# Performance work log

Measured on AMD Instinct MI355X. Metric: run time of the kernel, lower is better.

Reference implementation:

```python
import jax, jax.numpy as jnp
import numpy as np

N = 50000      # nodes
E = 800000     # edges (before self loops)
IN = 128       # in_channels
HID = 128      # 2*out_channels
OUT = 64       # out_channels
NEG_SLOPE = 0.2


def _gat_conv(x, src, dst, W, a_src, a_dst, b, n_nodes):
    """Single-head PyG GATConv (concat=True, heads=1, self-loops already added)."""
    h = x @ W                                   # [N, F]
    alpha_s = h @ a_src                         # [N]
    alpha_d = h @ a_dst                         # [N]
    e = alpha_s[src] + alpha_d[dst]             # [E'] logits per edge j->i
    e = jnp.where(e > 0, e, NEG_SLOPE * e)      # LeakyReLU(0.2)
    # segment softmax over destination node
    m = jax.ops.segment_max(e, dst, num_segments=n_nodes)   # [N]
    w = jnp.exp(e - m[dst])                                   # [E']
    denom = jax.ops.segment_sum(w, dst, num_segments=n_nodes) # [N]
    alpha = w / denom[dst]                                     # [E']
    out = jax.ops.segment_sum(alpha[:, None] * h[src], dst, num_segments=n_nodes)
    return out + b


def _with_self_loops(edge_index, n_nodes):
    loop = jnp.arange(n_nodes, dtype=edge_index.dtype)
    src = jnp.concatenate([edge_index[0], loop])
    dst = jnp.concatenate([edge_index[1], loop])
    return src, dst


def setup_inputs() -> dict:
    key = jax.random.key(0)
    ks = jax.random.split(key, 10)
    s = 0.1
    return {
        "x": jax.random.normal(ks[0], (N, IN), jnp.float32),
        "edge_index": jax.random.randint(ks[1], (2, E), 0, N, jnp.int32),
        "W1": jax.random.normal(ks[2], (IN, HID), jnp.float32) * s,
        "a1_src": jax.random.normal(ks[3], (HID,), jnp.float32) * s,
        "a1_dst": jax.random.normal(ks[4], (HID,), jnp.float32) * s,
        "b1": jnp.zeros((HID,), jnp.float32),
        "W2": jax.random.normal(ks[5], (HID, OUT), jnp.float32) * s,
        "a2_src": jax.random.normal(ks[6], (OUT,), jnp.float32) * s,
        "a2_dst": jax.random.normal(ks[7], (OUT,), jnp.float32) * s,
        "b2": jnp.zeros((OUT,), jnp.float32),
    }


def reference(x, edge_index, W1, a1_src, a1_dst, b1, W2, a2_src, a2_dst, b2):
    src, dst = _with_self_loops(edge_index, N)
    h = _gat_conv(x, src, dst, W1, a1_src, a1_dst, b1, N)
    h = jax.nn.relu(h)
    return _gat_conv(h, src, dst, W2, a2_src, a2_dst, b2, N)
```

## Files before the change

### kernel.cpp

```cpp
#include <hip/hip_runtime.h>
#include <hip/hip_bf16.h>


#define BCAP 4096

typedef __attribute__((ext_vector_type(8))) short bf16x8;
typedef __attribute__((ext_vector_type(4))) float f32x4;

__device__ __forceinline__ unsigned short bf16bits(float f){
  __hip_bfloat16 b = __float2bfloat16(f);
  return *(unsigned short*)&b;
}
__device__ __forceinline__ float bf16lo(unsigned int v){ return __uint_as_float(v << 16); }
__device__ __forceinline__ float bf16hi(unsigned int v){ return __uint_as_float(v & 0xFFFF0000u); }

__global__ __launch_bounds__(256) void prep_all(
    const float* __restrict__ W1, const float* __restrict__ W2,
    const float* __restrict__ a2s, const float* __restrict__ a2d,
    unsigned short* __restrict__ W1t, unsigned short* __restrict__ W2t,
    float* __restrict__ vas, float* __restrict__ vad,
    int* __restrict__ bucketCount)
{
  int b = blockIdx.x, t = threadIdx.x;
  if (b < 48){
    int idx = b*256 + t;
    if (idx < 8192){
      int n = idx >> 6, k2 = idx & 63;
      float a = W1[(size_t)(2*k2)*128 + n];
      float c = W1[(size_t)(2*k2+1)*128 + n];
      ushort2 o; o.x = bf16bits(a); o.y = bf16bits(c);
      *(ushort2*)&W1t[(size_t)n*128 + 2*k2] = o;
    } else {
      int r = idx - 8192;
      int n = r >> 6, k2 = r & 63;
      float a = W2[(size_t)(2*k2)*64 + n];
      float c = W2[(size_t)(2*k2+1)*64 + n];
      ushort2 o; o.x = bf16bits(a); o.y = bf16bits(c);
      *(ushort2*)&W2t[(size_t)n*128 + 2*k2] = o;
    }
  } else if (b == 48){
    int k = t & 127;
    const float* av = (t < 128) ? a2s : a2d;
    float* ov = (t < 128) ? vas : vad;
    float s = 0.f;
    for (int n=0; n<64; n++) s += W2[(size_t)k*64 + n] * av[n];
    ov[k] = s;
  } else {
    bucketCount[t] = 0; bucketCount[t+256] = 0;
  }
}

template<int NC, bool FUSE>
__device__ __forceinline__ void gemm_body(
    const float* __restrict__ Af, const unsigned short* __restrict__ Ah,
    const unsigned short* __restrict__ Wt,
    const float* __restrict__ avs, const float* __restrict__ avd,
    unsigned short* __restrict__ H, float* __restrict__ as_, float* __restrict__ ad_,
    int M, int rowBase, unsigned short* As, unsigned short* Ws)
{
  const int K = 128;
  int t = threadIdx.x;
  if (Af){
    #pragma unroll
    for (int i=0;i<8;i++){
      int idx = t + i*256; int r = idx>>5, k4 = idx&31;
      int grow = rowBase + r;
      float4 v = (grow<M) ? *(const float4*)&Af[(size_t)grow*K + k4*4]
                          : make_float4(0.f,0.f,0.f,0.f);
      ushort4 o; o.x=bf16bits(v.x); o.y=bf16bits(v.y); o.z=bf16bits(v.z); o.w=bf16bits(v.w);
      *(ushort4*)&As[r*136 + k4*4] = o;
    }
  } else {
    #pragma unroll
    for (int i=0;i<4;i++){
      int idx = t + i*256; int r = idx>>4, k8 = idx&15;
      int grow = rowBase + r;
      uint4 v = (grow<M) ? *(const uint4*)&Ah[(size_t)grow*K + k8*8]
                         : make_uint4(0u,0u,0u,0u);
      *(uint4*)&As[r*136 + k8*8] = v;
    }
  }
  int wave = t>>6, lane = t&63, ln = lane&15, q = lane>>4;
  f32x4 acc[NC/16];
  #pragma unroll
  for (int nt=0; nt<NC/16; nt++) acc[nt] = (f32x4){0.f,0.f,0.f,0.f};

  #pragma unroll
  for (int ch=0; ch<NC/64; ++ch){
    __syncthreads();
    #pragma unroll
    for (int i=0;i<4;i++){
      int idx = t + i*256; int n = idx>>4, k8 = idx&15;
      *(uint4*)&Ws[n*136 + k8*8] = *(const uint4*)&Wt[(size_t)(ch*64+n)*K + k8*8];
    }
    __syncthreads();
    #pragma unroll
    for (int kk=0;kk<4;kk++){
      bf16x8 a = *(const bf16x8*)&As[(wave*16+ln)*136 + kk*32 + q*8];
      #pragma unroll
      for (int nt=0; nt<4; nt++){
        bf16x8 b = *(const bf16x8*)&Ws[(nt*16+ln)*136 + kk*32 + q*8];
        acc[ch*4+nt] = __builtin_amdgcn_mfma_f32_16x16x32_bf16(a, b, acc[ch*4+nt], 0, 0, 0);
      }
    }
  }
  float asl[NC/16], adl[NC/16];
  if (FUSE){
    #pragma unroll
    for (int nt=0; nt<NC/16; nt++){ asl[nt]=avs[nt*16+ln]; adl[nt]=avd[nt*16+ln]; }
  }
  #pragma unroll
  for (int i=0;i<4;i++){
    int grow = rowBase + wave*16 + q*4 + i;
    if (grow < M){
      float ps=0.f, pd=0.f;
      #pragma unroll
      for (int nt=0; nt<NC/16; nt++){
        float v = acc[nt][i];
        H[(size_t)grow*NC + nt*16 + ln] = bf16bits(v);
        if (FUSE){ ps += v*asl[nt]; pd += v*adl[nt]; }
      }
      if (FUSE){
        #pragma unroll
        for (int d=1; d<16; d<<=1){ ps += __shfl_xor(ps,d); pd += __shfl_xor(pd,d); }
        if (ln==0){ as_[grow] = ps; ad_[grow] = pd; }
      }
    }
  }
}

__global__ __launch_bounds__(256) void scatter_or_gemm(
    const int* __restrict__ src, const int* __restrict__ dst,
    int* __restrict__ bucketCount, unsigned int* __restrict__ gbuf, int E, int SB,
    const float* __restrict__ x, const unsigned short* __restrict__ W1t,
    const float* __restrict__ a1s, const float* __restrict__ a1d,
    unsigned short* __restrict__ h1, float* __restrict__ as1, float* __restrict__ ad1,
    int M)
{
  __shared__ unsigned short smem[64*136 + 64*136];
  int t = threadIdx.x;
  if ((int)blockIdx.x >= SB){
    gemm_body<128, true>(x, nullptr, W1t, a1s, a1d, h1, as1, ad1, M,
                         (blockIdx.x - SB)*64, smem, smem + 64*136);
    return;
  }
  int* hist = (int*)smem;
  int* base = hist + 512;
  int e0 = blockIdx.x * 4096;
  hist[t] = 0; hist[t+256] = 0;
  __syncthreads();
  int sv[16], dv[16];
  #pragma unroll
  for (int k=0;k<16;k++){
    int i = e0 + t + k*256;
    if (i < E){ sv[k]=src[i]; dv[k]=dst[i]; atomicAdd(&hist[dv[k]>>7], 1); }
    else { sv[k] = -1; dv[k] = 0; }
  }
  __syncthreads();
  int h0 = hist[t], h1c = hist[t+256];
  if (h0 > 0)  base[t]     = atomicAdd(&bucketCount[t],     h0);
  if (h1c > 0) base[t+256] = atomicAdd(&bucketCount[t+256], h1c);
  __syncthreads();
  hist[t] = 0; hist[t+256] = 0;
  __syncthreads();
  #pragma unroll
  for (int k=0;k<16;k++){
    if (sv[k] >= 0){
      int b = dv[k] >> 7;
      int r = base[b] + atomicAdd(&hist[b], 1);
      if (r < BCAP)
        gbuf[(size_t)b*BCAP + r] = ((unsigned)(dv[k] & 127) << 16) | (unsigned)sv[k];
    }
  }
}

__global__ __launch_bounds__(512) void fine_sort(
    const unsigned int* __restrict__ gbuf, const int* __restrict__ bucketCount,
    int* __restrict__ offs, int* __restrict__ srcS, int N, int E, int B)
{
  __shared__ int sh[512];
  __shared__ int h[128];
  __shared__ int pre[128];
  __shared__ int rank[128];
  int b = blockIdx.x, t = threadIdx.x;
  {
    int nd_t = 0;
    if (t < B){ int lo=t*128; nd_t = (N-lo<128)?(N-lo):128; }
    sh[t] = (t < B ? bucketCount[t] : 0) + nd_t;
    __syncthreads();
    for (int d=1; d<512; d<<=1){
      int x = (t >= d) ? sh[t-d] : 0;
      __syncthreads();
      sh[t] += x;
      __syncthreads();
    }
  }
  int cnt = bucketCount[b]; if (cnt > BCAP) cnt = BCAP;
  int lo = b*128;
  int nd = (N - lo < 128) ? (N - lo) : 128;
  int base = sh[b] - (cnt + nd);
  if (b == 0 && t == 0) offs[N] = E + N;
  if (t < 128){ h[t] = 0; rank[t] = 0; }
  __syncthreads();
  for (int i = t; i < cnt; i += 512)
    atomicAdd(&h[(gbuf[(size_t)b*BCAP + i] >> 16) & 127], 1);
  __syncthreads();
  if (t < 128) pre[t] = (t < nd) ? (h[t] + 1) : 0;
  __syncthreads();
  for (int d=1; d<128; d<<=1){
    int x = (t >= d && t < 128) ? pre[t-d] : 0;
    __syncthreads();
    if (t < 128) pre[t] += x;
    __syncthreads();
  }
  int seg = (t < nd) ? (h[t] + 1) : 0;
  int ex  = (t < 128) ? (pre[t] - seg) : 0;
  if (t < nd){
    offs[lo + t] = base + ex;
    srcS[base + ex] = lo + t;
  }
  __syncthreads();
  if (t < 128) pre[t] = ex;
  __syncthreads();
  for (int i = t; i < cnt; i += 512){
    unsigned e = gbuf[(size_t)b*BCAP + i];
    int dl = (e >> 16) & 127;
    int s  = e & 0xFFFF;
    int r  = atomicAdd(&rank[dl], 1);
    srcS[base + pre[dl] + 1 + r] = s;
  }
}

__global__ __launch_bounds__(256) void edge_agg128(
    const int* __restrict__ offs, const int* __restrict__ srcS,
    const float* __restrict__ asrc, const float* __restrict__ adst,
    const unsigned short* __restrict__ Hin, const float* __restrict__ bias,
    unsigned short* __restrict__ outp,
    const float* __restrict__ vas, const float* __restrict__ vad,
    float* __restrict__ as2, float* __restrict__ ad2, int n)
{
  int wid  = (blockIdx.x * 256 + threadIdx.x) >> 6;
  int lane = threadIdx.x & 63;
  if (wid >= n) return;
  int beg = offs[wid], end = offs[wid+1];
  float ad = adst[wid];
  int qw = lane >> 4, ql = lane & 15;
  float acc[8] = {}; float denom = 0.f;
  for (int base = beg; base < end; base += 64){
    int m = end - base; if (m > 64) m = 64;
    int   sv = (lane < m) ? srcS[base + lane] : 0;
    float av = (lane < m) ? asrc[sv] : 0.f;
    float ev = av + ad;
    ev = (ev > 0.f) ? ev : 0.2f*ev;
    float wv = (lane < m) ? __expf(ev) : 0.f;
    int j = 0;
    for (; j + 16 <= m; j += 16){
      int i0 = j+qw, i1 = j+4+qw, i2 = j+8+qw, i3 = j+12+qw;
      int   s0 = __shfl(sv,i0), s1 = __shfl(sv,i1), s2 = __shfl(sv,i2), s3 = __shfl(sv,i3);
      float w0 = __shfl(wv,i0), w1 = __shfl(wv,i1), w2 = __shfl(wv,i2), w3 = __shfl(wv,i3);
      uint4 ha = *(const uint4*)&Hin[(size_t)s0*128 + ql*8];
      uint4 hb = *(const uint4*)&Hin[(size_t)s1*128 + ql*8];
      uint4 hc = *(const uint4*)&Hin[(size_t)s2*128 + ql*8];
      uint4 hd = *(const uint4*)&Hin[(size_t)s3*128 + ql*8];
      denom += (w0 + w1) + (w2 + w3);
      acc[0]+=w0*bf16lo(ha.x)+w1*bf16lo(hb.x)+w2*bf16lo(hc.x)+w3*bf16lo(hd.x);
      acc[1]+=w0*bf16hi(ha.x)+w1*bf16hi(hb.x)+w2*bf16hi(hc.x)+w3*bf16hi(hd.x);
      acc[2]+=w0*bf16lo(ha.y)+w1*bf16lo(hb.y)+w2*bf16lo(hc.y)+w3*bf16lo(hd.y);
      acc[3]+=w0*bf16hi(ha.y)+w1*bf16hi(hb.y)+w2*bf16hi(hc.y)+w3*bf16hi(hd.y);
      acc[4]+=w0*bf16lo(ha.z)+w1*bf16lo(hb.z)+w2*bf16lo(hc.z)+w3*bf16lo(hd.z);
      acc[5]+=w0*bf16hi(ha.z)+w1*bf16hi(hb.z)+w2*bf16hi(hc.z)+w3*bf16hi(hd.z);
      acc[6]+=w0*bf16lo(ha.w)+w1*bf16lo(hb.w)+w2*bf16lo(hc.w)+w3*bf16lo(hd.w);
      acc[7]+=w0*bf16hi(ha.w)+w1*bf16hi(hb.w)+w2*bf16hi(hc.w)+w3*bf16hi(hd.w);
    }
    for (; j < m; j += 4){
      int i0 = j + qw;
      int   s0 = __shfl(sv, i0);
      float w0 = __shfl(wv, i0);
      uint4 ha = *(const uint4*)&Hin[(size_t)s0*128 + ql*8];
      denom += w0;
      acc[0]+=w0*bf16lo(ha.x); acc[1]+=w0*bf16hi(ha.x);
      acc[2]+=w0*bf16lo(ha.y); acc[3]+=w0*bf16hi(ha.y);
      acc[4]+=w0*bf16lo(ha.z); acc[5]+=w0*bf16hi(ha.z);
      acc[6]+=w0*bf16lo(ha.w); acc[7]+=w0*bf16hi(ha.w);
    }
  }
  denom += __shfl_xor(denom,16); denom += __shfl_xor(denom,32);
  #pragma unroll
  for (int k=0;k<8;k++){ acc[k]+=__shfl_xor(acc[k],16); acc[k]+=__shfl_xor(acc[k],32); }
  if (qw == 0){
    float inv = 1.0f / denom;
    float ps = 0.f, pd = 0.f;
    unsigned short o[8];
    #pragma unroll
    for (int k=0;k<8;k++){
      float v = fmaxf(acc[k]*inv + bias[ql*8+k], 0.f);
      o[k] = bf16bits(v);
      ps += v * vas[ql*8+k];
      pd += v * vad[ql*8+k];
    }
    *(uint4*)&outp[(size_t)wid*128 + ql*8] = *(uint4*)o;
    #pragma unroll
    for (int d=1; d<16; d<<=1){ ps += __shfl_xor(ps,d); pd += __shfl_xor(pd,d); }
    if (ql == 0){ as2[wid] = ps; ad2[wid] = pd; }
  }
}

__global__ __launch_bounds__(256) void gemm2_k(
    const unsigned short* __restrict__ A, const unsigned short* __restrict__ Wt,
    unsigned short* __restrict__ H, int M)
{
  __shared__ unsigned short smem[64*136 + 64*136];
  gemm_body<64, false>(nullptr, A, Wt, nullptr, nullptr, H, nullptr, nullptr,
                       M, blockIdx.x*64, smem, smem + 64*136);
}

__global__ __launch_bounds__(256) void edge_agg64(
    const int* __restrict__ offs, const int* __restrict__ srcS,
    const float* __restrict__ asrc, const float* __restrict__ adst,
    const unsigned short* __restrict__ Hin, const float* __restrict__ bias,
    float* __restrict__ outp, int n)
{
  int wid  = (blockIdx.x * 256 + threadIdx.x) >> 6;
  int lane = threadIdx.x & 63;
  if (wid >= n) return;
  int beg = offs[wid], end = offs[wid+1];
  float ad = adst[wid];
  int ew = lane >> 3, el = lane & 7;
  float acc[8] = {}; float denom = 0.f;
  for (int base = beg; base < end; base += 64){
    int m = end - base; if (m > 64) m = 64;
    int   sv = (lane < m) ? srcS[base + lane] : 0;
    float av = (lane < m) ? asrc[sv] : 0.f;
    float ev = av + ad;
    ev = (ev > 0.f) ? ev : 0.2f*ev;
    float wv = (lane < m) ? __expf(ev) : 0.f;
    int j = 0;
    for (; j + 32 <= m; j += 32){
      int i0 = j+ew, i1 = j+8+ew, i2 = j+16+ew, i3 = j+24+ew;
      int   s0 = __shfl(sv,i0), s1 = __shfl(sv,i1), s2 = __shfl(sv,i2), s3 = __shfl(sv,i3);
      float w0 = __shfl(wv,i0), w1 = __shfl(wv,i1), w2 = __shfl(wv,i2), w3 = __shfl(wv,i3);
      uint4 ha = *(const uint4*)&Hin[(size_t)s0*64 + el*8];
      uint4 hb = *(const uint4*)&Hin[(size_t)s1*64 + el*8];
      uint4 hc = *(const uint4*)&Hin[(size_t)s2*64 + el*8];
      uint4 hd = *(const uint4*)&Hin[(size_t)s3*64 + el*8];
      denom += (w0 + w1) + (w2 + w3);
      acc[0]+=w0*bf16lo(ha.x)+w1*bf16lo(hb.x)+w2*bf16lo(hc.x)+w3*bf16lo(hd.x);
      acc[1]+=w0*bf16hi(ha.x)+w1*bf16hi(hb.x)+w2*bf16hi(hc.x)+w3*bf16hi(hd.x);
      acc[2]+=w0*bf16lo(ha.y)+w1*bf16lo(hb.y)+w2*bf16lo(hc.y)+w3*bf16lo(hd.y);
      acc[3]+=w0*bf16hi(ha.y)+w1*bf16hi(hb.y)+w2*bf16hi(hc.y)+w3*bf16hi(hd.y);
      acc[4]+=w0*bf16lo(ha.z)+w1*bf16lo(hb.z)+w2*bf16lo(hc.z)+w3*bf16lo(hd.z);
      acc[5]+=w0*bf16hi(ha.z)+w1*bf16hi(hb.z)+w2*bf16hi(hc.z)+w3*bf16hi(hd.z);
      acc[6]+=w0*bf16lo(ha.w)+w1*bf16lo(hb.w)+w2*bf16lo(hc.w)+w3*bf16lo(hd.w);
      acc[7]+=w0*bf16hi(ha.w)+w1*bf16hi(hb.w)+w2*bf16hi(hc.w)+w3*bf16hi(hd.w);
    }
    for (; j < m; j += 8){
      int i0 = j + ew;
      int   s0 = __shfl(sv, i0);
      float w0 = __shfl(wv, i0);
      uint4 ha = *(const uint4*)&Hin[(size_t)s0*64 + el*8];
      denom += w0;
      acc[0]+=w0*bf16lo(ha.x); acc[1]+=w0*bf16hi(ha.x);
      acc[2]+=w0*bf16lo(ha.y); acc[3]+=w0*bf16hi(ha.y);
      acc[4]+=w0*bf16lo(ha.z); acc[5]+=w0*bf16hi(ha.z);
      acc[6]+=w0*bf16lo(ha.w); acc[7]+=w0*bf16hi(ha.w);
    }
  }
  denom += __shfl_xor(denom,8); denom += __shfl_xor(denom,16); denom += __shfl_xor(denom,32);
  #pragma unroll
  for (int k=0;k<8;k++){
    acc[k]+=__shfl_xor(acc[k],8); acc[k]+=__shfl_xor(acc[k],16); acc[k]+=__shfl_xor(acc[k],32);
  }
  if (ew == 0){
    float inv = 1.0f / denom;
    float4 o0, o1;
    o0.x = acc[0]*inv + bias[el*8+0]; o0.y = acc[1]*inv + bias[el*8+1];
    o0.z = acc[2]*inv + bias[el*8+2]; o0.w = acc[3]*inv + bias[el*8+3];
    o1.x = acc[4]*inv + bias[el*8+4]; o1.y = acc[5]*inv + bias[el*8+5];
    o1.z = acc[6]*inv + bias[el*8+6]; o1.w = acc[7]*inv + bias[el*8+7];
    *(float4*)&outp[(size_t)wid*64 + el*8]     = o0;
    *(float4*)&outp[(size_t)wid*64 + el*8 + 4] = o1;
  }
}

extern "C" void kernel_launch(void* const* d_in, const int* in_sizes, int n_in,
                              void* d_out, int out_size, void* d_ws, size_t ws_size,
                              hipStream_t stream) {
  const int IN = 128, HID = 128, OUT = 64;
  const int N = in_sizes[0] / IN;
  const int E = in_sizes[1] / 2;
  const int B = (N + 127) / 128;
  const int SB = (E + 4095) / 4096;

  const float* x    = (const float*)d_in[0];
  const int*   ei   = (const int*)d_in[1];
  const float* W1   = (const float*)d_in[2];
  const float* a1s  = (const float*)d_in[3];
  const float* a1d  = (const float*)d_in[4];
  const float* b1   = (const float*)d_in[5];
  const float* W2   = (const float*)d_in[6];
  const float* a2s  = (const float*)d_in[7];
  const float* a2d  = (const float*)d_in[8];
  const float* b2   = (const float*)d_in[9];
  float* out = (float*)d_out;

  char* w = (char*)d_ws;
  unsigned short* W1t = (unsigned short*)w; w += (size_t)HID*IN*2;
  unsigned short* W2t = (unsigned short*)w; w += (size_t)OUT*HID*2;
  unsigned short* h1    = (unsigned short*)w; w += (size_t)N*128*2;
  unsigned short* hrelu = (unsigned short*)w; w += (size_t)N*128*2;
  unsigned short* h2 = h1;
  float* as1   = (float*)w; w += (size_t)N*4;
  float* ad1   = (float*)w; w += (size_t)N*4;
  float* as2   = (float*)w; w += (size_t)N*4;
  float* ad2   = (float*)w; w += (size_t)N*4;
  float* vas   = (float*)w; w += 128*4;
  float* vad   = (float*)w; w += 128*4;
  int* offs    = (int*)w;   w += (size_t)(N+1)*4;
  int* bucketCount = (int*)w; w += 512*4;
  int* srcS    = (int*)w;   w += (size_t)(E+N)*4;
  unsigned int* gbuf = (unsigned int*)w; w += (size_t)B*BCAP*4;

  const int* esrc = ei;
  const int* edst = ei + E;

  hipLaunchKernelGGL(prep_all, dim3(50), dim3(256), 0, stream,
                     W1, W2, a2s, a2d, W1t, W2t, vas, vad, bucketCount);
  hipLaunchKernelGGL(scatter_or_gemm, dim3(SB + (N+63)/64), dim3(256), 0, stream,
                     esrc, edst, bucketCount, gbuf, E, SB,
                     x, W1t, a1s, a1d, h1, as1, ad1, N);
  hipLaunchKernelGGL(fine_sort, dim3(B), dim3(512), 0, stream,
                     gbuf, bucketCount, offs, srcS, N, E, B);
  hipLaunchKernelGGL(edge_agg128, dim3((N*64+255)/256), dim3(256), 0, stream,
                     offs, srcS, as1, ad1, h1, b1, hrelu, vas, vad, as2, ad2, N);
  hipLaunchKernelGGL(gemm2_k, dim3((N+63)/64), dim3(256), 0, stream,
                     hrelu, W2t, h2, N);
  hipLaunchKernelGGL(edge_agg64, dim3((N*64+255)/256), dim3(256), 0, stream,
                     offs, srcS, as2, ad2, h2, b2, out, N);
}
```

Measured before the change: 192.1 us.

## Stage neighbor feature rows into LDS via global_load_lds in edge aggregation

Both edge aggregation kernels now issue all neighbor feature-row gathers for a 32-edge chunk as direct global-to-LDS loads into a per-wave staging buffer, wait once, then read the rows from LDS for the weighted accumulation. The aim is to get many gathers in flight at once and take VGPR pressure off the load path, hiding random-access latency. The chunk size drops from 64 to 32 edges, and the denominator is now a full-wave reduction of per-lane weights. The cost is extra LDS traffic, LDS footprint that may limit occupancy, and a hard wait per chunk that serialises load and compute.

After: 195.6 us. No clear change (+1.8%).

```diff
diff --git a/kernel.cpp b/kernel.cpp
--- a/kernel.cpp
+++ b/kernel.cpp
@@ -13,6 +13,12 @@
 }
 __device__ __forceinline__ float bf16lo(unsigned int v){ return __uint_as_float(v << 16); }
 __device__ __forceinline__ float bf16hi(unsigned int v){ return __uint_as_float(v & 0xFFFF0000u); }
+
+__device__ __forceinline__ void gload_lds16(const void* g, void* l){
+  __builtin_amdgcn_global_load_lds(
+      (const __attribute__((address_space(1))) void*)g,
+      (__attribute__((address_space(3))) void*)l, 16, 0, 0);
+}
 
 __global__ __launch_bounds__(256) void prep_all(
     const float* __restrict__ W1, const float* __restrict__ W2,
@@ -239,30 +245,43 @@
     const float* __restrict__ vas, const float* __restrict__ vad,
     float* __restrict__ as2, float* __restrict__ ad2, int n)
 {
+  __shared__ alignas(16) unsigned short stg[4][8*512];
   int wid  = (blockIdx.x * 256 + threadIdx.x) >> 6;
   int lane = threadIdx.x & 63;
   if (wid >= n) return;
+  int wslot = __builtin_amdgcn_readfirstlane((threadIdx.x >> 6) & 3);
+  unsigned short* my = &stg[wslot][0];
   int beg = offs[wid], end = offs[wid+1];
   float ad = adst[wid];
   int qw = lane >> 4, ql = lane & 15;
-  float acc[8] = {}; float denom = 0.f;
-  for (int base = beg; base < end; base += 64){
-    int m = end - base; if (m > 64) m = 64;
-    int   sv = (lane < m) ? srcS[base + lane] : 0;
-    float av = (lane < m) ? asrc[sv] : 0.f;
-    float ev = av + ad;
-    ev = (ev > 0.f) ? ev : 0.2f*ev;
-    float wv = (lane < m) ? __expf(ev) : 0.f;
+  float acc[8] = {}; float dn = 0.f;
+  for (int base = beg; base < end; base += 32){
+    int m = end - base; if (m > 32) m = 32;
+    int sv = 0; float wv = 0.f;
+    if (lane < m){
+      sv = srcS[base + lane];
+      float ev = asrc[sv] + ad;
+      ev = (ev > 0.f) ? ev : 0.2f*ev;
+      wv = __expf(ev);
+    }
+    dn += wv;
+    asm volatile("s_waitcnt lgkmcnt(0)" ::: "memory");
+    #pragma unroll
+    for (int i = 0; i < 8; i++){
+      if (i*4 < m){
+        int s = __shfl(sv, i*4 + qw);
+        gload_lds16(&Hin[(size_t)s*128 + ql*8], &my[i*512]);
+      }
+    }
+    asm volatile("s_waitcnt vmcnt(0)" ::: "memory");
     int j = 0;
     for (; j + 16 <= m; j += 16){
-      int i0 = j+qw, i1 = j+4+qw, i2 = j+8+qw, i3 = j+12+qw;
-      int   s0 = __shfl(sv,i0), s1 = __shfl(sv,i1), s2 = __shfl(sv,i2), s3 = __shfl(sv,i3);
-      float w0 = __shfl(wv,i0), w1 = __shfl(wv,i1), w2 = __shfl(wv,i2), w3 = __shfl(wv,i3);
-      uint4 ha = *(const uint4*)&Hin[(size_t)s0*128 + ql*8];
-      uint4 hb = *(const uint4*)&Hin[(size_t)s1*128 + ql*8];
-      uint4 hc = *(const uint4*)&Hin[(size_t)s2*128 + ql*8];
-      uint4 hd = *(const uint4*)&Hin[(size_t)s3*128 + ql*8];
-      denom += (w0 + w1) + (w2 + w3);
+      uint4 ha = *(const uint4*)&my[(j+qw)*128    + ql*8];
+      uint4 hb = *(const uint4*)&my[(j+4+qw)*128  + ql*8];
+      uint4 hc = *(const uint4*)&my[(j+8+qw)*128  + ql*8];
+      uint4 hd = *(const uint4*)&my[(j+12+qw)*128 + ql*8];
+      float w0 = __shfl(wv, j+qw),   w1 = __shfl(wv, j+4+qw);
+      float w2 = __shfl(wv, j+8+qw), w3 = __shfl(wv, j+12+qw);
       acc[0]+=w0*bf16lo(ha.x)+w1*bf16lo(hb.x)+w2*bf16lo(hc.x)+w3*bf16lo(hd.x);
       acc[1]+=w0*bf16hi(ha.x)+w1*bf16hi(hb.x)+w2*bf16hi(hc.x)+w3*bf16hi(hd.x);
       acc[2]+=w0*bf16lo(ha.y)+w1*bf16lo(hb.y)+w2*bf16lo(hc.y)+w3*bf16lo(hd.y);
@@ -273,22 +292,20 @@
       acc[7]+=w0*bf16hi(ha.w)+w1*bf16hi(hb.w)+w2*bf16hi(hc.w)+w3*bf16hi(hd.w);
     }
     for (; j < m; j += 4){
-      int i0 = j + qw;
-      int   s0 = __shfl(sv, i0);
-      float w0 = __shfl(wv, i0);
-      uint4 ha = *(const uint4*)&Hin[(size_t)s0*128 + ql*8];
-      denom += w0;
+      uint4 ha = *(const uint4*)&my[(j+qw)*128 + ql*8];
+      float w0 = __shfl(wv, j+qw);
       acc[0]+=w0*bf16lo(ha.x); acc[1]+=w0*bf16hi(ha.x);
       acc[2]+=w0*bf16lo(ha.y); acc[3]+=w0*bf16hi(ha.y);
       acc[4]+=w0*bf16lo(ha.z); acc[5]+=w0*bf16hi(ha.z);
       acc[6]+=w0*bf16lo(ha.w); acc[7]+=w0*bf16hi(ha.w);
     }
   }
-  denom += __shfl_xor(denom,16); denom += __shfl_xor(denom,32);
+  #pragma unroll
+  for (int d=1; d<64; d<<=1) dn += __shfl_xor(dn, d);
   #pragma unroll
   for (int k=0;k<8;k++){ acc[k]+=__shfl_xor(acc[k],16); acc[k]+=__shfl_xor(acc[k],32); }
   if (qw == 0){
-    float inv = 1.0f / denom;
+    float inv = 1.0f / dn;
     float ps = 0.f, pd = 0.f;
     unsigned short o[8];
     #pragma unroll
@@ -320,58 +337,66 @@
     const unsigned short* __restrict__ Hin, const float* __restrict__ bias,
     float* __restrict__ outp, int n)
 {
+  __shared__ alignas(16) unsigned short stg[4][4*512];
   int wid  = (blockIdx.x * 256 + threadIdx.x) >> 6;
   int lane = threadIdx.x & 63;
   if (wid >= n) return;
+  int wslot = __builtin_amdgcn_readfirstlane((threadIdx.x >> 6) & 3);
+  unsigned short* my = &stg[wslot][0];
   int beg = offs[wid], end = offs[wid+1];
   float ad = adst[wid];
   int ew = lane >> 3, el = lane & 7;
-  float acc[8] = {}; float denom = 0.f;
-  for (int base = beg; base < end; base += 64){
-    int m = end - base; if (m > 64) m = 64;
-    int   sv = (lane < m) ? srcS[base + lane] : 0;
-    float av = (lane < m) ? asrc[sv] : 0.f;
-    float ev = av + ad;
-    ev = (ev > 0.f) ? ev : 0.2f*ev;
-    float wv = (lane < m) ? __expf(ev) : 0.f;
+  float acc[8] = {}; float dn = 0.f;
+  for (int base = beg; base < end; base += 32){
+    int m = end - base; if (m > 32) m = 32;
+    int sv = 0; float wv = 0.f;
+    if (lane < m){
+      sv = srcS[base + lane];
+      float ev = asrc[sv] + ad;
+      ev = (ev > 0.f) ? ev : 0.2f*ev;
+      wv = __expf(ev);
+    }
+    dn += wv;
+    asm volatile("s_waitcnt lgkmcnt(0)" ::: "memory");
+    #pragma unroll
+    for (int i = 0; i < 4; i++){
+      if (i*8 < m){
+        int s = __shfl(sv, i*8 + ew);
+        gload_lds16(&Hin[(size_t)s*64 + el*8], &my[i*512]);
+      }
+    }
+    asm volatile("s_waitcnt vmcnt(0)" ::: "memory");
     int j = 0;
-    for (; j + 32 <= m; j += 32){
-      int i0 = j+ew, i1 = j+8+ew, i2 = j+16+ew, i3 = j+24+ew;
-      int   s0 = __shfl(sv,i0), s1 = __shfl(sv,i1), s2 = __shfl(sv,i2), s3 = __shfl(sv,i3);
-      float w0 = __shfl(wv,i0), w1 = __shfl(wv,i1), w2 = __shfl(wv,i2), w3 = __shfl(wv,i3);
-      uint4 ha = *(const uint4*)&Hin[(size_t)s0*64 + el*8];
-      uint4 hb = *(const uint4*)&Hin[(size_t)s1*64 + el*8];
-      uint4 hc = *(const uint4*)&Hin[(size_t)s2*64 + el*8];
-      uint4 hd = *(const uint4*)&Hin[(size_t)s3*64 + el*8];
-      denom += (w0 + w1) + (w2 + w3);
-      acc[0]+=w0*bf16lo(ha.x)+w1*bf16lo(hb.x)+w2*bf16lo(hc.x)+w3*bf16lo(hd.x);
-      acc[1]+=w0*bf16hi(ha.x)+w1*bf16hi(hb.x)+w2*bf16hi(hc.x)+w3*bf16hi(hd.x);
-      acc[2]+=w0*bf16lo(ha.y)+w1*bf16lo(hb.y)+w2*bf16lo(hc.y)+w3*bf16lo(hd.y);
-      acc[3]+=w0*bf16hi(ha.y)+w1*bf16hi(hb.y)+w2*bf16hi(hc.y)+w3*bf16hi(hd.y);
-      acc[4]+=w0*bf16lo(ha.z)+w1*bf16lo(hb.z)+w2*bf16lo(hc.z)+w3*bf16lo(hd.z);
-      acc[5]+=w0*bf16hi(ha.z)+w1*bf16hi(hb.z)+w2*bf16hi(hc.z)+w3*bf16hi(hd.z);
-      acc[6]+=w0*bf16lo(ha.w)+w1*bf16lo(hb.w)+w2*bf16lo(hc.w)+w3*bf16lo(hd.w);
-      acc[7]+=w0*bf16hi(ha.w)+w1*bf16hi(hb.w)+w2*bf16hi(hc.w)+w3*bf16hi(hd.w);
+    for (; j + 16 <= m; j += 16){
+      uint4 ha = *(const uint4*)&my[(j+ew)*64   + el*8];
+      uint4 hb = *(const uint4*)&my[(j+8+ew)*64 + el*8];
+      float w0 = __shfl(wv, j+ew), w1 = __shfl(wv, j+8+ew);
+      acc[0]+=w0*bf16lo(ha.x)+w1*bf16lo(hb.x);
+      acc[1]+=w0*bf16hi(ha.x)+w1*bf16hi(hb.x);
+      acc[2]+=w0*bf16lo(ha.y)+w1*bf16lo(hb.y);
+      acc[3]+=w0*bf16hi(ha.y)+w1*bf16hi(hb.y);
+      acc[4]+=w0*bf16lo(ha.z)+w1*bf16lo(hb.z);
+      acc[5]+=w0*bf16hi(ha.z)+w1*bf16hi(hb.z);
+      acc[6]+=w0*bf16lo(ha.w)+w1*bf16lo(hb.w);
+      acc[7]+=w0*bf16hi(ha.w)+w1*bf16hi(hb.w);
     }
     for (; j < m; j += 8){
-      int i0 = j + ew;
-      int   s0 = __shfl(sv, i0);
-      float w0 = __shfl(wv, i0);
-      uint4 ha = *(const uint4*)&Hin[(size_t)s0*64 + el*8];
-      denom += w0;
+      uint4 ha = *(const uint4*)&my[(j+ew)*64 + el*8];
+      float w0 = __shfl(wv, j+ew);
       acc[0]+=w0*bf16lo(ha.x); acc[1]+=w0*bf16hi(ha.x);
       acc[2]+=w0*bf16lo(ha.y); acc[3]+=w0*bf16hi(ha.y);
       acc[4]+=w0*bf16lo(ha.z); acc[5]+=w0*bf16hi(ha.z);
       acc[6]+=w0*bf16lo(ha.w); acc[7]+=w0*bf16hi(ha.w);
     }
   }
-  denom += __shfl_xor(denom,8); denom += __shfl_xor(denom,16); denom += __shfl_xor(denom,32);
+  #pragma unroll
+  for (int d=1; d<64; d<<=1) dn += __shfl_xor(dn, d);
   #pragma unroll
   for (int k=0;k<8;k++){
     acc[k]+=__shfl_xor(acc[k],8); acc[k]+=__shfl_xor(acc[k],16); acc[k]+=__shfl_xor(acc[k],32);
   }
   if (ew == 0){
-    float inv = 1.0f / denom;
+    float inv = 1.0f / dn;
     float4 o0, o1;
     o0.x = acc[0]*inv + bias[el*8+0]; o0.y = acc[1]*inv + bias[el*8+1];
     o0.z = acc[2]*inv + bias[el*8+2]; o0.w = acc[3]*inv + bias[el*8+3];
```
